# Performance work log

Measured on AMD Instinct MI355X. Metric: run time of the kernel, lower is better.

## Reference

```python
import jax, jax.numpy as jnp
import numpy as np
from jax import lax

ITERATIONS = 8
KT, KH, KW = 3, 7, 7


def _ssm_op(left, right):
    a1, b1 = left
    a2, b2 = right
    return (a1 * a2, a2 * b1 + b2)


def setup_inputs() -> dict:
    key = jax.random.key(0)
    k1, k2, k3 = jax.random.split(key, 3)
    B, T, H, W, C = 1, 16, 64, 64, 128
    x = jax.random.normal(k1, (B, T, H, W, C), dtype=jnp.float32)
    A_kernel = 0.02 * jax.random.normal(k2, (C, KT, KH, KW), dtype=jnp.float32)
    B_kernel = 0.02 * jax.random.normal(k3, (C, KT, KH, KW), dtype=jnp.float32)
    return {"x": x, "A_kernel": A_kernel, "B_kernel": B_kernel}


def _pad_kernel_fft(kern, T, H, W):
    # Place (C, kt, kh, kw) kernel circularly centered into a (C, T, H, W) canvas, FFT it.
    C = kern.shape[0]
    t_idx = (jnp.arange(KT) - KT // 2) % T
    h_idx = (jnp.arange(KH) - KH // 2) % H
    w_idx = (jnp.arange(KW) - KW // 2) % W
    tt, th, tw = jnp.meshgrid(t_idx, h_idx, w_idx, indexing="ij")
    padded = jnp.zeros((C, T, H, W), dtype=kern.dtype).at[:, tt, th, tw].set(kern)
    kf = jnp.fft.fftn(padded, axes=(1, 2, 3))  # (C, T, H, W) complex
    return kf.transpose(1, 2, 3, 0)[None, ...]  # (1, T, H, W, C)


def reference(x, A_kernel, B_kernel):
    B, T, H, W, C = x.shape
    A_stable = 0.9 * jnp.tanh(A_kernel)
    A_f = _pad_kernel_fft(A_stable, T, H, W)   # (1,T,H,W,C)
    B_f = _pad_kernel_fft(B_kernel, T, H, W)   # (1,T,H,W,C)
    x_f = jnp.fft.fftn(x, axes=(1, 2, 3))      # (B,T,H,W,C)
    Bx_f = B_f * x_f
    a_seq = jnp.broadcast_to(A_f, (ITERATIONS, B, T, H, W, C))
    b_seq = jnp.broadcast_to(Bx_f, (ITERATIONS, B, T, H, W, C))
    _, h_all_f = lax.associative_scan(_ssm_op, (a_seq, b_seq), axis=0)
    h_final = jnp.fft.ifftn(h_all_f[-1], axes=(1, 2, 3)).real
    return h_final
```

## Files before the change

kernel.cpp:

```cpp
#include <hip/hip_runtime.h>
#include <hip/hip_fp16.h>
#include <math.h>

#define TT 16
#define HH 64
#define WW 64
#define CC 128
#define PI2 6.283185307179586f

#define LROW(r) (((r) & 0x38) | ((((r) >> 3) ^ (r)) & 7))

__device__ __forceinline__ float2 cadd(float2 a, float2 b){ return make_float2(a.x+b.x, a.y+b.y); }
__device__ __forceinline__ float2 csub(float2 a, float2 b){ return make_float2(a.x-b.x, a.y-b.y); }
__device__ __forceinline__ float2 cmul(float2 a, float2 b) {
    return make_float2(a.x*b.x - a.y*b.y, a.x*b.y + a.y*b.x);
}
__device__ __forceinline__ float2 cmac(float2 acc, float2 a, float2 b) {
    acc.x = fmaf(a.x, b.x, fmaf(-a.y, b.y, acc.x));
    acc.y = fmaf(a.x, b.y, fmaf(a.y, b.x, acc.y));
    return acc;
}
__device__ __forceinline__ float2 csq(float2 a) {
    return make_float2(a.x*a.x - a.y*a.y, 2.f*a.x*a.y);
}

template<int SGN>
__device__ __forceinline__ void dft4(float2 b0, float2 b1, float2 b2, float2 b3,
                                     float2& y0, float2& y1, float2& y2, float2& y3) {
    float2 e0 = cadd(b0, b2), e1 = csub(b0, b2);
    float2 o0 = cadd(b1, b3), o1 = csub(b1, b3);
    y0 = cadd(e0, o0); y2 = csub(e0, o0);
    float2 r = make_float2((float)(-SGN) * o1.y, (float)SGN * o1.x);
    y1 = cadd(e1, r); y3 = csub(e1, r);
}

template<int SGN>
__device__ __forceinline__ void dft8(const float2* a, float2* X) {
    const float C = 0.70710678118654752f;
    float2 E0,E1,E2,E3,O0,O1,O2,O3;
    dft4<SGN>(a[0],a[2],a[4],a[6], E0,E1,E2,E3);
    dft4<SGN>(a[1],a[3],a[5],a[7], O0,O1,O2,O3);
    float2 T1 = make_float2(C*(O1.x - (float)SGN*O1.y), C*((float)SGN*O1.x + O1.y));
    float2 T2 = make_float2((float)(-SGN)*O2.y, (float)SGN*O2.x);
    float2 T3 = make_float2(-C*(O3.x + (float)SGN*O3.y), C*((float)SGN*O3.x - O3.y));
    X[0]=cadd(E0,O0); X[4]=csub(E0,O0);
    X[1]=cadd(E1,T1); X[5]=csub(E1,T1);
    X[2]=cadd(E2,T2); X[6]=csub(E2,T2);
    X[3]=cadd(E3,T3); X[7]=csub(E3,T3);
}

template<int SGN>
__device__ __forceinline__ void dft16(const float2* v, float2* X) {
    const float ct[10] = {1.f, 0.92387953251f, 0.70710678119f, 0.38268343236f, 0.f,
                          0.f, -0.70710678119f, 0.f, 0.f, -0.92387953251f};
    const float st[10] = {0.f, 0.38268343236f, 0.70710678119f, 0.92387953251f, 1.f,
                          0.f, 0.70710678119f, 0.f, 0.f, -0.38268343236f};
    float2 Z[16];
    #pragma unroll
    for (int h0 = 0; h0 < 4; ++h0) {
        float2 y0,y1,y2,y3;
        dft4<SGN>(v[h0], v[4+h0], v[8+h0], v[12+h0], y0,y1,y2,y3);
        float2 ys[4] = {y0,y1,y2,y3};
        #pragma unroll
        for (int k0 = 0; k0 < 4; ++k0) {
            int m = h0 * k0;
            float cc = ct[m], ss = (float)SGN * st[m];
            Z[k0*4 + h0] = make_float2(ys[k0].x*cc - ys[k0].y*ss,
                                       ys[k0].x*ss + ys[k0].y*cc);
        }
    }
    #pragma unroll
    for (int k0 = 0; k0 < 4; ++k0) {
        float2 y0,y1,y2,y3;
        dft4<SGN>(Z[k0*4+0], Z[k0*4+1], Z[k0*4+2], Z[k0*4+3], y0,y1,y2,y3);
        X[k0] = y0; X[k0+4] = y1; X[k0+8] = y2; X[k0+12] = y3;
    }
}


__global__ __launch_bounds__(256) void pA(const float* __restrict__ x,
                                          uint4* __restrict__ Z,
                                          const float* __restrict__ Ak,
                                          const float* __restrict__ Bk,
                                          __half2* __restrict__ Ahw,
                                          __half2* __restrict__ Bhw) {
    __shared__ __align__(16) char smem[32768];
    int bid = blockIdx.x;
    int tid = threadIdx.x;
    if (bid < 1024) {
        float (*zsre)[64][32] = (float(*)[64][32])smem;
        float (*zsim)[64][32] = (float(*)[64][32])(smem + 16384);
        float (*spre)[64][32] = (float(*)[64][32])smem;
        float (*spim)[64][32] = (float(*)[64][32])(smem + 16384);
        int cq = bid & 3, hq = (bid >> 2) & 15, t = bid >> 6;
        int c = tid & 31, s4 = tid >> 5;
        float twc[8], tws[8];
        {
            float s1, c1; sincosf(-PI2 * s4 / 64.0f, &s1, &c1);
            twc[0] = 1.f; tws[0] = 0.f;
            #pragma unroll
            for (int k = 1; k < 8; ++k) {
                twc[k] = twc[k-1]*c1 - tws[k-1]*s1;
                tws[k] = twc[k-1]*s1 + tws[k-1]*c1;
            }
        }
        const float* xb = x + (size_t)(t*64 + hq*4) * 8192 + cq * 32 + c;
        #pragma unroll
        for (int p = 0; p < 2; ++p) {
            float2 a[8], Y[8];
            #pragma unroll
            for (int h1 = 0; h1 < 8; ++h1) {
                size_t off = (size_t)(h1*8 + s4) * 128;
                a[h1] = make_float2(xb[(size_t)(2*p) * 8192 + off],
                                    xb[(size_t)(2*p+1) * 8192 + off]);
            }
            dft8<-1>(a, Y);
            #pragma unroll
            for (int k0 = 0; k0 < 8; ++k0) {
                int row = k0*8 + s4;
                zsre[p][row][c] = Y[k0].x*twc[k0] - Y[k0].y*tws[k0];
                zsim[p][row][c] = Y[k0].x*tws[k0] + Y[k0].y*twc[k0];
            }
        }
        __syncthreads();
        float2 X0[8], X1[8];
        {
            float2 b[8];
            #pragma unroll
            for (int h0 = 0; h0 < 8; ++h0)
                b[h0] = make_float2(zsre[0][s4*8 + h0][c], zsim[0][s4*8 + h0][c]);
            dft8<-1>(b, X0);
            #pragma unroll
            for (int h0 = 0; h0 < 8; ++h0)
                b[h0] = make_float2(zsre[1][s4*8 + h0][c], zsim[1][s4*8 + h0][c]);
            dft8<-1>(b, X1);
        }
        __syncthreads();
        #pragma unroll
        for (int k1 = 0; k1 < 8; ++k1) {
            int row = s4 + 8*k1;
            spre[0][row][c] = X0[k1].x; spim[0][row][c] = X0[k1].y;
            spre[1][row][c] = X1[k1].x; spim[1][row][c] = X1[k1].y;
        }
        __syncthreads();
        for (int i = tid; i < 528; i += 256) {
            int p = i & 1, ccl = (i >> 1) & 7, om = i >> 4;
            int mo = (64 - om) & 63;
            uint4 u1, u2;
            unsigned int* p1o = &u1.x;
            unsigned int* p2o = &u2.x;
            #pragma unroll
            for (int j = 0; j < 4; ++j) {
                int cb = ccl*4 + j;
                float2 za = make_float2(spre[p][om][cb], spim[p][om][cb]);
                float2 zb = make_float2(spre[p][mo][cb], spim[p][mo][cb]);
                float2 Xa = make_float2(0.5f*(za.x + zb.x), 0.5f*(za.y - zb.y));
                float2 Xb = make_float2(0.5f*(za.y + zb.y), 0.5f*(zb.x - za.x));
                __half2 h1v = __float22half2_rn(Xa);
                __half2 h2v = __float22half2_rn(Xb);
                p1o[j] = *(unsigned int*)&h1v;
                p2o[j] = *(unsigned int*)&h2v;
            }
            size_t base = ((size_t)(om*32 + cq*8 + ccl)*16 + t)*64 + hq*4;
            Z[base + 2*p]     = u1;
            Z[base + 2*p + 1] = u2;
        }
    } else {
        float (*Asl)[7][64] = (float(*)[7][64])smem;
        float (*Bsl)[7][64] = (float(*)[7][64])(smem + 12544);
        float2 (*Awl)[64]   = (float2(*)[64])(smem + 25088);
        float2 (*Bwl)[64]   = (float2(*)[64])(smem + 28672);
        float2* tw64        = (float2*)(smem + 32256);
        int kid = bid - 1024;
        int kt = kid / 66;
        int rem = kid % 66;
        int om = rem >> 1, chalf = rem & 1;
        int c0 = chalf * 64;
        for (int i = tid; i < 64; i += 256) {
            float s, cw; sincosf(-PI2 * i / 64.0f, &s, &cw);
            tw64[i] = make_float2(cw, s);
        }
        for (int i = tid; i < 49 * 64; i += 256) {
            int p = i >> 6, cl = i & 63;
            int kh = p / 7, kw = p % 7;
            int idx = (((c0 + cl) * 3 + kt) * 7 + kh) * 7 + kw;
            Asl[kh][kw][cl] = 0.9f * tanhf(Ak[idx]);
            Bsl[kh][kw][cl] = Bk[idx];
        }
        __syncthreads();
        for (int i = tid; i < 7 * 64; i += 256) {
            int kh = i >> 6, cl = i & 63;
            float2 aA = make_float2(0.f,0.f), aB = make_float2(0.f,0.f);
            #pragma unroll
            for (int kw = 0; kw < 7; ++kw) {
                float2 tw = tw64[(om * (kw - 3)) & 63];
                float va = Asl[kh][kw][cl], vb = Bsl[kh][kw][cl];
                aA.x = fmaf(va, tw.x, aA.x); aA.y = fmaf(va, tw.y, aA.y);
                aB.x = fmaf(vb, tw.x, aB.x); aB.y = fmaf(vb, tw.y, aB.y);
            }
            Awl[kh][cl] = aA; Bwl[kh][cl] = aB;
        }
        __syncthreads();
        for (int i = tid; i < 64 * 64; i += 256) {
            int eta = i >> 6, cl = i & 63;
            float2 aA = make_float2(0.f,0.f), aB = make_float2(0.f,0.f);
            #pragma unroll
            for (int kh = 0; kh < 7; ++kh) {
                float2 tw = tw64[(eta * (kh - 3)) & 63];
                aA = cmac(aA, Awl[kh][cl], tw);
                aB = cmac(aB, Bwl[kh][cl], tw);
            }
            int ep = ((eta & 7) << 3) | (eta >> 3);
            int o = ((kt * 33 + om) * 64 + ep) * 128 + c0 + cl;
            Ahw[o] = __float22half2_rn(aA);
            Bhw[o] = __float22half2_rn(aB);
        }
    }
}

__global__ __launch_bounds__(256) void pmid(uint4* __restrict__ Z,
                                            const __half2* __restrict__ Ahw,
                                            const __half2* __restrict__ Bhw) {
    __shared__ float tre[16][64][4];
    __shared__ float tim[16][64][4];
    int l = (blockIdx.x & 7) * 132 + (blockIdx.x >> 3);
    int om = l >> 5, cc = l & 31;
    int c0 = cc * 4;
    int tid = threadIdx.x;
    uint4* g = Z + (size_t)l * 1024;

    int d = tid & 7;
    float twc[8], tws[8];
    {
        float s1, c1; sincosf(-PI2 * d / 64.0f, &s1, &c1);
        twc[0] = 1.f; tws[0] = 0.f;
        #pragma unroll
        for (int k = 1; k < 8; ++k) {
            twc[k] = twc[k-1]*c1 - tws[k-1]*s1;
            tws[k] = twc[k-1]*s1 + tws[k-1]*c1;
        }
    }
    for (int i = tid; i < 1024; i += 256) {
        uint4 u = g[i];
        int t = i >> 6, h = i & 63;
        int pr = LROW(h);
        float2 v0 = __half22float2(*(__half2*)&u.x);
        float2 v1 = __half22float2(*(__half2*)&u.y);
        float2 v2 = __half22float2(*(__half2*)&u.z);
        float2 v3 = __half22float2(*(__half2*)&u.w);
        tre[t][pr][0] = v0.x; tim[t][pr][0] = v0.y;
        tre[t][pr][1] = v1.x; tim[t][pr][1] = v1.y;
        tre[t][pr][2] = v2.x; tim[t][pr][2] = v2.y;
        tre[t][pr][3] = v3.x; tim[t][pr][3] = v3.y;
    }
    __syncthreads();
    int cl = (tid >> 3) & 3, ts = tid >> 5;
    #pragma unroll
    for (int q = 0; q < 2; ++q) {
        int t = ts*2 + q;
        float2 a[8], Y[8];
        #pragma unroll
        for (int h1 = 0; h1 < 8; ++h1) {
            int pr = LROW(h1*8 + d);
            a[h1] = make_float2(tre[t][pr][cl], tim[t][pr][cl]);
        }
        dft8<-1>(a, Y);
        #pragma unroll
        for (int k0 = 0; k0 < 8; ++k0) {
            int pr = LROW(k0*8 + d);
            tre[t][pr][cl] = Y[k0].x*twc[k0] - Y[k0].y*tws[k0];
            tim[t][pr][cl] = Y[k0].x*tws[k0] + Y[k0].y*twc[k0];
        }
    }
    __syncthreads();
    #pragma unroll
    for (int q = 0; q < 2; ++q) {
        int t = ts*2 + q;
        float2 a[8], Y[8];
        #pragma unroll
        for (int h0 = 0; h0 < 8; ++h0) {
            int pr = LROW(d*8 + h0);
            a[h0] = make_float2(tre[t][pr][cl], tim[t][pr][cl]);
        }
        dft8<-1>(a, Y);
        #pragma unroll
        for (int k1 = 0; k1 < 8; ++k1) {
            int pr = LROW(d*8 + k1);
            tre[t][pr][cl] = Y[k1].x; tim[t][pr][cl] = Y[k1].y;
        }
    }
    __syncthreads();
    {
        const float CT16[16] = {1.f, 0.9238795325f, 0.7071067812f, 0.3826834324f, 0.f,
                                -0.3826834324f, -0.7071067812f, -0.9238795325f, -1.f,
                                -0.9238795325f, -0.7071067812f, -0.3826834324f, 0.f,
                                0.3826834324f, 0.7071067812f, 0.9238795325f};
        const float ST16[16] = {0.f, 0.3826834324f, 0.7071067812f, 0.9238795325f, 1.f,
                                0.9238795325f, 0.7071067812f, 0.3826834324f, 0.f,
                                -0.3826834324f, -0.7071067812f, -0.9238795325f, -1.f,
                                -0.9238795325f, -0.7071067812f, -0.3826834324f};
        int cg = tid & 3, rT = tid >> 2;
        const int PKT = 33 * 64 * 128;
        int kb = (om * 64 + rT) * 128 + c0 + cg;
        float2 A0 = __half22float2(Ahw[kb]);
        float2 A1 = __half22float2(Ahw[kb + PKT]);
        float2 A2 = __half22float2(Ahw[kb + 2*PKT]);
        float2 B0 = __half22float2(Bhw[kb]);
        float2 B1 = __half22float2(Bhw[kb + PKT]);
        float2 B2 = __half22float2(Bhw[kb + 2*PKT]);
        int pr = LROW(rT);
        float2 v[16], X[16];
        #pragma unroll
        for (int t = 0; t < 16; ++t) v[t] = make_float2(tre[t][pr][cg], tim[t][pr][cg]);
        dft16<-1>(v, X);
        #pragma unroll
        for (int ta = 0; ta < 16; ++ta) {
            float2 wv = make_float2(CT16[ta], -ST16[ta]);
            float2 wc = make_float2(CT16[ta],  ST16[ta]);
            float2 Af = A1; Af = cmac(Af, A0, wc); Af = cmac(Af, A2, wv);
            float2 Bf = B1; Bf = cmac(Bf, B0, wc); Bf = cmac(Bf, B2, wv);
            float2 A2q = csq(Af), A4q = csq(A2q);
            float2 S = cmul(make_float2(1.f+Af.x, Af.y), make_float2(1.f+A2q.x, A2q.y));
            S = cmul(S, make_float2(1.f+A4q.x, A4q.y));
            float2 G = cmul(S, Bf);
            X[ta] = cmul(X[ta], G);
        }
        dft16<1>(X, v);
        const float sc = 0.015625f;
        #pragma unroll
        for (int t = 0; t < 16; ++t) {
            tre[t][pr][cg] = v[t].x * sc;
            tim[t][pr][cg] = v[t].y * sc;
        }
    }
    __syncthreads();
    #pragma unroll
    for (int q = 0; q < 2; ++q) {
        int t = ts*2 + q;
        float2 a[8], Y[8];
        #pragma unroll
        for (int e1 = 0; e1 < 8; ++e1) {
            int pr = LROW(d*8 + e1);
            a[e1] = make_float2(tre[t][pr][cl], tim[t][pr][cl]);
        }
        dft8<1>(a, Y);
        #pragma unroll
        for (int h0 = 0; h0 < 8; ++h0) {
            int pr = LROW(d*8 + h0);
            tre[t][pr][cl] =  Y[h0].x*twc[h0] + Y[h0].y*tws[h0];
            tim[t][pr][cl] = -Y[h0].x*tws[h0] + Y[h0].y*twc[h0];
        }
    }
    __syncthreads();
    #pragma unroll
    for (int q = 0; q < 2; ++q) {
        int t = ts*2 + q;
        float2 a[8], Y[8];
        #pragma unroll
        for (int e0 = 0; e0 < 8; ++e0) {
            int pr = LROW(e0*8 + d);
            a[e0] = make_float2(tre[t][pr][cl], tim[t][pr][cl]);
        }
        dft8<1>(a, Y);
        #pragma unroll
        for (int h1 = 0; h1 < 8; ++h1) {
            int pr = LROW(d + 8*h1);
            tre[t][pr][cl] = Y[h1].x; tim[t][pr][cl] = Y[h1].y;
        }
    }
    __syncthreads();
    for (int i = tid; i < 1024; i += 256) {
        int t = i >> 6, h = i & 63;
        int pr = LROW(h);
        uint4 u;
        __half2 v0 = __float22half2_rn(make_float2(tre[t][pr][0], tim[t][pr][0]));
        __half2 v1 = __float22half2_rn(make_float2(tre[t][pr][1], tim[t][pr][1]));
        __half2 v2 = __float22half2_rn(make_float2(tre[t][pr][2], tim[t][pr][2]));
        __half2 v3 = __float22half2_rn(make_float2(tre[t][pr][3], tim[t][pr][3]));
        u.x = *(unsigned int*)&v0; u.y = *(unsigned int*)&v1;
        u.z = *(unsigned int*)&v2; u.w = *(unsigned int*)&v3;
        g[i] = u;
    }
}

__global__ __launch_bounds__(256) void p5(const uint4* __restrict__ Z,
                                          float* __restrict__ out) {
    __shared__ float plre[2][64][32];
    __shared__ float plim[2][64][32];
    __shared__ float2 tw64[64];
    int bid = blockIdx.x;
    int cq = bid & 3, hq = (bid >> 2) & 15, t = bid >> 6;
    int tid = threadIdx.x;
    if (tid < 64) {
        float s, cw; sincosf(PI2 * tid / 64.0f, &s, &cw);
        tw64[tid] = make_float2(cw, s);
    }
    for (int i = tid; i < 528; i += 256) {
        int p = i & 1, ccl = (i >> 1) & 7, om = i >> 4;
        size_t base = ((size_t)(om*32 + cq*8 + ccl)*16 + t)*64 + hq*4;
        uint4 ua = Z[base + 2*p];
        uint4 ub = Z[base + 2*p + 1];
        const unsigned int* pa = &ua.x;
        const unsigned int* pb = &ub.x;
        #pragma unroll
        for (int j = 0; j < 4; ++j) {
            float2 za = __half22float2(*(const __half2*)&pa[j]);
            float2 zb = __half22float2(*(const __half2*)&pb[j]);
            plre[p][om][ccl*4+j] = za.x - zb.y;
            plim[p][om][ccl*4+j] = za.y + zb.x;
            if (om >= 1 && om <= 31) {
                plre[p][64-om][ccl*4+j] = za.x + zb.y;
                plim[p][64-om][ccl*4+j] = zb.x - za.y;
            }
        }
    }
    __syncthreads();
    int c = tid & 31, s4 = tid >> 5;
    float2 ar[2][8];
    #pragma unroll
    for (int p = 0; p < 2; ++p)
        #pragma unroll
        for (int h1 = 0; h1 < 8; ++h1)
            ar[p][h1] = make_float2(plre[p][h1*8 + s4][c], plim[p][h1*8 + s4][c]);
    __syncthreads();
    #pragma unroll
    for (int p = 0; p < 2; ++p) {
        float2 Y[8];
        dft8<1>(ar[p], Y);
        #pragma unroll
        for (int k0 = 0; k0 < 8; ++k0) {
            float2 z = cmul(Y[k0], tw64[(s4 * k0) & 63]);
            plre[p][k0*8 + s4][c] = z.x;
            plim[p][k0*8 + s4][c] = z.y;
        }
    }
    __syncthreads();
    #pragma unroll
    for (int p = 0; p < 2; ++p) {
        float2 b[8], X[8];
        #pragma unroll
        for (int h0 = 0; h0 < 8; ++h0)
            b[h0] = make_float2(plre[p][s4*8 + h0][c], plim[p][s4*8 + h0][c]);
        dft8<1>(b, X);
        float* dst = out + (size_t)(t*64 + hq*4 + 2*p) * 8192 + cq * 32 + c;
        #pragma unroll
        for (int k1 = 0; k1 < 8; ++k1) {
            size_t o = (size_t)(s4 + 8*k1) * 128;
            dst[o]        = X[k1].x * (1.0f / 1024.0f);
            dst[o + 8192] = X[k1].y * (1.0f / 1024.0f);
        }
    }
}

extern "C" void kernel_launch(void* const* d_in, const int* in_sizes, int n_in,
                              void* d_out, int out_size, void* d_ws, size_t ws_size,
                              hipStream_t stream) {
    const float* x  = (const float*)d_in[0];
    const float* Ak = (const float*)d_in[1];
    const float* Bk = (const float*)d_in[2];
    float* out = (float*)d_out;

    uint4* Z = (uint4*)d_ws;
    __half2* Ahw = (__half2*)((char*)d_ws + (size_t)33*32*1024*16);
    __half2* Bhw = Ahw + 3 * 33 * 64 * 128;

    hipLaunchKernelGGL(pA,   dim3(1222), dim3(256), 0, stream, x, Z, Ak, Bk, Ahw, Bhw);
    hipLaunchKernelGGL(pmid, dim3(1056), dim3(256), 0, stream, Z, Ahw, Bhw);
    hipLaunchKernelGGL(p5,   dim3(1024), dim3(256), 0, stream, Z, out);
}
```

Before: 56.93 us.

## Precompute full spectral filter G in kernel-prep blocks instead of in pmid

Kernel-prep blocks now handle all three temporal taps for one (om, channel half, eta half), apply the time-axis DFT of the kernel, and evaluate the geometric-series filter G = (1+A)(1+A^2)(1+A^4)B for all 16 temporal frequencies. They store G as half2 in a layout pmid can read with four vector loads per thread. This removes the per-element filter arithmetic and six scattered half2 loads from pmid, whose prefetch is also issued early to overlap with the FFT stages. In exchange the prep blocks do more work each (132 instead of 198) and the G buffer is larger, so the prep tail could lengthen.

Result: slower. 88.82 us (+56.0%).

```diff
diff --git a/kernel.cpp b/kernel.cpp
--- a/kernel.cpp
+++ b/kernel.cpp
@@ -82,9 +82,8 @@
                                           uint4* __restrict__ Z,
                                           const float* __restrict__ Ak,
                                           const float* __restrict__ Bk,
-                                          __half2* __restrict__ Ahw,
-                                          __half2* __restrict__ Bhw) {
-    __shared__ __align__(16) char smem[32768];
+                                          __half2* __restrict__ Ghw) {
+    __shared__ __align__(16) char smem[36352];
     int bid = blockIdx.x;
     int tid = threadIdx.x;
     if (bid < 1024) {
@@ -166,61 +165,85 @@
             Z[base + 2*p + 1] = u2;
         }
     } else {
-        float (*Asl)[7][64] = (float(*)[7][64])smem;
-        float (*Bsl)[7][64] = (float(*)[7][64])(smem + 12544);
-        float2 (*Awl)[64]   = (float2(*)[64])(smem + 25088);
-        float2 (*Bwl)[64]   = (float2(*)[64])(smem + 28672);
-        float2* tw64        = (float2*)(smem + 32256);
+        float (*Asl)[7][64]   = (float(*)[7][64])smem;
+        float (*Bsl)[7][64]   = (float(*)[7][64])(smem + 12544);
+        __half2 (*Awl)[7][64] = (__half2(*)[7][64])(smem + 25088);
+        __half2 (*Bwl)[7][64] = (__half2(*)[7][64])(smem + 30464);
+        float2* tw64          = (float2*)(smem + 35840);
         int kid = bid - 1024;
-        int kt = kid / 66;
-        int rem = kid % 66;
-        int om = rem >> 1, chalf = rem & 1;
+        int eh = kid & 1, chalf = (kid >> 1) & 1, om = kid >> 2;
         int c0 = chalf * 64;
         for (int i = tid; i < 64; i += 256) {
             float s, cw; sincosf(-PI2 * i / 64.0f, &s, &cw);
             tw64[i] = make_float2(cw, s);
         }
-        for (int i = tid; i < 49 * 64; i += 256) {
-            int p = i >> 6, cl = i & 63;
-            int kh = p / 7, kw = p % 7;
-            int idx = (((c0 + cl) * 3 + kt) * 7 + kh) * 7 + kw;
-            Asl[kh][kw][cl] = 0.9f * tanhf(Ak[idx]);
-            Bsl[kh][kw][cl] = Bk[idx];
-        }
         __syncthreads();
-        for (int i = tid; i < 7 * 64; i += 256) {
-            int kh = i >> 6, cl = i & 63;
-            float2 aA = make_float2(0.f,0.f), aB = make_float2(0.f,0.f);
-            #pragma unroll
-            for (int kw = 0; kw < 7; ++kw) {
-                float2 tw = tw64[(om * (kw - 3)) & 63];
-                float va = Asl[kh][kw][cl], vb = Bsl[kh][kw][cl];
-                aA.x = fmaf(va, tw.x, aA.x); aA.y = fmaf(va, tw.y, aA.y);
-                aB.x = fmaf(vb, tw.x, aB.x); aB.y = fmaf(vb, tw.y, aB.y);
-            }
-            Awl[kh][cl] = aA; Bwl[kh][cl] = aB;
-        }
-        __syncthreads();
-        for (int i = tid; i < 64 * 64; i += 256) {
-            int eta = i >> 6, cl = i & 63;
-            float2 aA = make_float2(0.f,0.f), aB = make_float2(0.f,0.f);
+        for (int kt = 0; kt < 3; ++kt) {
+            for (int i = tid; i < 49 * 64; i += 256) {
+                int p = i >> 6, cl = i & 63;
+                int kh = p / 7, kw = p % 7;
+                int idx = (((c0 + cl) * 3 + kt) * 7 + kh) * 7 + kw;
+                Asl[kh][kw][cl] = 0.9f * tanhf(Ak[idx]);
+                Bsl[kh][kw][cl] = Bk[idx];
+            }
+            __syncthreads();
+            for (int i = tid; i < 7 * 64; i += 256) {
+                int kh = i >> 6, cl = i & 63;
+                float2 aA = make_float2(0.f,0.f), aB = make_float2(0.f,0.f);
+                #pragma unroll
+                for (int kw = 0; kw < 7; ++kw) {
+                    float2 tw = tw64[(om * (kw - 3)) & 63];
+                    float va = Asl[kh][kw][cl], vb = Bsl[kh][kw][cl];
+                    aA.x = fmaf(va, tw.x, aA.x); aA.y = fmaf(va, tw.y, aA.y);
+                    aB.x = fmaf(vb, tw.x, aB.x); aB.y = fmaf(vb, tw.y, aB.y);
+                }
+                Awl[kt][kh][cl] = __float22half2_rn(aA);
+                Bwl[kt][kh][cl] = __float22half2_rn(aB);
+            }
+            __syncthreads();
+        }
+        const float CT16[16] = {1.f, 0.9238795325f, 0.7071067812f, 0.3826834324f, 0.f,
+                                -0.3826834324f, -0.7071067812f, -0.9238795325f, -1.f,
+                                -0.9238795325f, -0.7071067812f, -0.3826834324f, 0.f,
+                                0.3826834324f, 0.7071067812f, 0.9238795325f};
+        const float ST16[16] = {0.f, 0.3826834324f, 0.7071067812f, 0.9238795325f, 1.f,
+                                0.9238795325f, 0.7071067812f, 0.3826834324f, 0.f,
+                                -0.3826834324f, -0.7071067812f, -0.9238795325f, -1.f,
+                                -0.9238795325f, -0.7071067812f, -0.3826834324f};
+        for (int i = tid; i < 32 * 64; i += 256) {
+            int eta = eh * 32 + (i >> 6), cl = i & 63;
+            float2 A0 = make_float2(0.f,0.f), A1 = A0, A2 = A0;
+            float2 B0 = A0, B1 = A0, B2 = A0;
             #pragma unroll
             for (int kh = 0; kh < 7; ++kh) {
                 float2 tw = tw64[(eta * (kh - 3)) & 63];
-                aA = cmac(aA, Awl[kh][cl], tw);
-                aB = cmac(aB, Bwl[kh][cl], tw);
+                A0 = cmac(A0, __half22float2(Awl[0][kh][cl]), tw);
+                A1 = cmac(A1, __half22float2(Awl[1][kh][cl]), tw);
+                A2 = cmac(A2, __half22float2(Awl[2][kh][cl]), tw);
+                B0 = cmac(B0, __half22float2(Bwl[0][kh][cl]), tw);
+                B1 = cmac(B1, __half22float2(Bwl[1][kh][cl]), tw);
+                B2 = cmac(B2, __half22float2(Bwl[2][kh][cl]), tw);
             }
             int ep = ((eta & 7) << 3) | (eta >> 3);
-            int o = ((kt * 33 + om) * 64 + ep) * 128 + c0 + cl;
-            Ahw[o] = __float22half2_rn(aA);
-            Bhw[o] = __float22half2_rn(aB);
+            size_t gb = ((size_t)(om*64 + ep)*128 + c0 + cl) * 16;
+            #pragma unroll
+            for (int ta = 0; ta < 16; ++ta) {
+                float2 wv = make_float2(CT16[ta], -ST16[ta]);
+                float2 wc = make_float2(CT16[ta],  ST16[ta]);
+                float2 Af = A1; Af = cmac(Af, A0, wc); Af = cmac(Af, A2, wv);
+                float2 Bf = B1; Bf = cmac(Bf, B0, wc); Bf = cmac(Bf, B2, wv);
+                float2 A2q = csq(Af), A4q = csq(A2q);
+                float2 S = cmul(make_float2(1.f+Af.x, Af.y), make_float2(1.f+A2q.x, A2q.y));
+                S = cmul(S, make_float2(1.f+A4q.x, A4q.y));
+                float2 G = cmul(S, Bf);
+                Ghw[gb + ta] = __float22half2_rn(G);
+            }
         }
     }
 }
 
 __global__ __launch_bounds__(256) void pmid(uint4* __restrict__ Z,
-                                            const __half2* __restrict__ Ahw,
-                                            const __half2* __restrict__ Bhw) {
+                                            const __half2* __restrict__ Ghw) {
     __shared__ float tre[16][64][4];
     __shared__ float tim[16][64][4];
     int l = (blockIdx.x & 7) * 132 + (blockIdx.x >> 3);
@@ -228,6 +251,10 @@
     int c0 = cc * 4;
     int tid = threadIdx.x;
     uint4* g = Z + (size_t)l * 1024;
+
+    int cg = tid & 3, rT = tid >> 2;
+    const uint4* Gp = (const uint4*)(Ghw + ((size_t)(om*64 + rT)*128 + c0 + cg)*16);
+    uint4 gq0 = Gp[0], gq1 = Gp[1], gq2 = Gp[2], gq3 = Gp[3];
 
     int d = tid & 7;
     float twc[8], tws[8];
@@ -291,38 +318,20 @@
     }
     __syncthreads();
     {
-        const float CT16[16] = {1.f, 0.9238795325f, 0.7071067812f, 0.3826834324f, 0.f,
-                                -0.3826834324f, -0.7071067812f, -0.9238795325f, -1.f,
-                                -0.9238795325f, -0.7071067812f, -0.3826834324f, 0.f,
-                                0.3826834324f, 0.7071067812f, 0.9238795325f};
-        const float ST16[16] = {0.f, 0.3826834324f, 0.7071067812f, 0.9238795325f, 1.f,
-                                0.9238795325f, 0.7071067812f, 0.3826834324f, 0.f,
-                                -0.3826834324f, -0.7071067812f, -0.9238795325f, -1.f,
-                                -0.9238795325f, -0.7071067812f, -0.3826834324f};
-        int cg = tid & 3, rT = tid >> 2;
-        const int PKT = 33 * 64 * 128;
-        int kb = (om * 64 + rT) * 128 + c0 + cg;
-        float2 A0 = __half22float2(Ahw[kb]);
-        float2 A1 = __half22float2(Ahw[kb + PKT]);
-        float2 A2 = __half22float2(Ahw[kb + 2*PKT]);
-        float2 B0 = __half22float2(Bhw[kb]);
-        float2 B1 = __half22float2(Bhw[kb + PKT]);
-        float2 B2 = __half22float2(Bhw[kb + 2*PKT]);
         int pr = LROW(rT);
         float2 v[16], X[16];
         #pragma unroll
         for (int t = 0; t < 16; ++t) v[t] = make_float2(tre[t][pr][cg], tim[t][pr][cg]);
         dft16<-1>(v, X);
+        const unsigned int* gw = &gq0.x;
+        unsigned int gwa[16] = {gq0.x, gq0.y, gq0.z, gq0.w,
+                                gq1.x, gq1.y, gq1.z, gq1.w,
+                                gq2.x, gq2.y, gq2.z, gq2.w,
+                                gq3.x, gq3.y, gq3.z, gq3.w};
+        (void)gw;
         #pragma unroll
         for (int ta = 0; ta < 16; ++ta) {
-            float2 wv = make_float2(CT16[ta], -ST16[ta]);
-            float2 wc = make_float2(CT16[ta],  ST16[ta]);
-            float2 Af = A1; Af = cmac(Af, A0, wc); Af = cmac(Af, A2, wv);
-            float2 Bf = B1; Bf = cmac(Bf, B0, wc); Bf = cmac(Bf, B2, wv);
-            float2 A2q = csq(Af), A4q = csq(A2q);
-            float2 S = cmul(make_float2(1.f+Af.x, Af.y), make_float2(1.f+A2q.x, A2q.y));
-            S = cmul(S, make_float2(1.f+A4q.x, A4q.y));
-            float2 G = cmul(S, Bf);
+            float2 G = __half22float2(*(const __half2*)&gwa[ta]);
             X[ta] = cmul(X[ta], G);
         }
         dft16<1>(X, v);
@@ -461,10 +470,9 @@
     float* out = (float*)d_out;
 
     uint4* Z = (uint4*)d_ws;
-    __half2* Ahw = (__half2*)((char*)d_ws + (size_t)33*32*1024*16);
-    __half2* Bhw = Ahw + 3 * 33 * 64 * 128;
-
-    hipLaunchKernelGGL(pA,   dim3(1222), dim3(256), 0, stream, x, Z, Ak, Bk, Ahw, Bhw);
-    hipLaunchKernelGGL(pmid, dim3(1056), dim3(256), 0, stream, Z, Ahw, Bhw);
+    __half2* Ghw = (__half2*)((char*)d_ws + (size_t)33*32*1024*16);
+
+    hipLaunchKernelGGL(pA,   dim3(1156), dim3(256), 0, stream, x, Z, Ak, Bk, Ghw);
+    hipLaunchKernelGGL(pmid, dim3(1056), dim3(256), 0, stream, Z, Ghw);
     hipLaunchKernelGGL(p5,   dim3(1024), dim3(256), 0, stream, Z, out);
 }
```
